# Performance work log

Measured on AMD Instinct MI355X. Metric: run time of the kernel, lower is better.

The kernel has to match this reference:

```python
import jax, jax.numpy as jnp
import numpy as np

E = 1024   # embedding_dim
H = 16     # heads
W = 1024   # lag / seq length
B = 4      # batch
D = E // H # head dim


def setup_inputs() -> dict:
    key = jax.random.key(0)
    ks = jax.random.split(key, 5)
    scale = E ** -0.5
    return {
        "x":   jax.random.normal(ks[0], (3, B, E, W), dtype=jnp.float32),
        "L_Q": jax.random.normal(ks[1], (E, E), dtype=jnp.float32) * scale,
        "L_K": jax.random.normal(ks[2], (E, E), dtype=jnp.float32) * scale,
        "L_V": jax.random.normal(ks[3], (E, E), dtype=jnp.float32) * scale,
        "M":   jax.random.normal(ks[4], (E, E), dtype=jnp.float32) * (1.0 / (2 * E)) ** 0.5,
        "b":   jnp.zeros((E, 1), dtype=jnp.float32),
    }


def reference(x, L_Q, L_K, L_V, M, b):
    # x: [3, B, E, W] channels-first; x[0]=K input, x[1]=Q input, x[2]=V input
    K = jnp.einsum('ef,bfw->bew', L_K, x[0])
    Q = jnp.einsum('ef,bfw->bew', L_Q, x[1])
    V = jnp.einsum('ef,bfw->bew', L_V, x[2])
    # reshape to [B, H, D, W]
    Kv = K.reshape(B, H, D, W)
    Qv = Q.reshape(B, H, D, W)
    Vv = V.reshape(B, H, D, W)
    # scores[b,h,q,k] = Q_v^T @ K_v
    scores = jnp.einsum('bhdq,bhdk->bhqk', Qv, Kv)
    # causal mask: -inf for q > k (strictly lower triangle), added BEFORE softmax
    q_idx = jnp.arange(W)[:, None]
    k_idx = jnp.arange(W)[None, :]
    mask = jnp.where(q_idx > k_idx, -jnp.inf, 0.0).astype(scores.dtype)
    scores = scores + mask
    # NON-STANDARD: softmax over the QUERY axis (dim=-2), then scale
    attn = jax.nn.softmax(scores, axis=-2) / (E ** 0.5)
    # V_v @ scores: [B,H,D,W] @ [B,H,W,W] -> [B,H,D,W]
    out = jnp.einsum('bhdq,bhqk->bhdk', Vv, attn).reshape(B, E, W)
    # dense: M @ out + b (dropout identity at inference)
    return jnp.einsum('oe,bew->bow', M, out) + b
```

## Files before the change

### kernel.cpp

```cpp
#include <hip/hip_runtime.h>
#include <stdint.h>
#include <math.h>

#define E_DIM 1024
#define W_DIM 1024
#define EW 1048576L

typedef _Float16 h16;
typedef __attribute__((ext_vector_type(8))) _Float16 h8;
typedef __attribute__((ext_vector_type(4))) float f4;

__device__ __forceinline__ void async_copy16(h16* lds, const h16* g) {
    __builtin_amdgcn_global_load_lds(
        (const __attribute__((address_space(1))) void*)g,
        (__attribute__((address_space(3))) void*)lds, 16, 0, 0);
}

__global__ __launch_bounds__(256) void prep(
    const float* __restrict__ x, const float* __restrict__ LK,
    const float* __restrict__ LQ, const float* __restrict__ LV,
    const float* __restrict__ Mw, h16* __restrict__ xt, h16* __restrict__ wh)
{
    __shared__ float Ts[64][65];
    const int z = blockIdx.z;
    const int t = threadIdx.x;
    if (z < 12) {
        const float* src = x + (long)z * EW;
        h16* dst = xt + (long)z * EW;
        const int e0 = blockIdx.y * 64, w0 = blockIdx.x * 64;
        const int r = t >> 4, c4 = (t & 15) * 4;
        #pragma unroll
        for (int p = 0; p < 4; ++p) {
            float4 v = *reinterpret_cast<const float4*>(src + (long)(e0 + r + p * 16) * W_DIM + w0 + c4);
            Ts[c4 + 0][r + p * 16] = v.x;
            Ts[c4 + 1][r + p * 16] = v.y;
            Ts[c4 + 2][r + p * 16] = v.z;
            Ts[c4 + 3][r + p * 16] = v.w;
        }
        __syncthreads();
        #pragma unroll
        for (int p = 0; p < 4; ++p) {
            int wr = r + p * 16;
            union { h16 h[4]; uint2 u; } o;
            o.h[0] = (h16)Ts[wr][c4 + 0];
            o.h[1] = (h16)Ts[wr][c4 + 1];
            o.h[2] = (h16)Ts[wr][c4 + 2];
            o.h[3] = (h16)Ts[wr][c4 + 3];
            *reinterpret_cast<uint2*>(dst + (long)(w0 + wr) * E_DIM + e0 + c4) = o.u;
        }
    } else {
        const float* srcs[4] = {LK, LQ, LV, Mw};
        const float* s = srcs[z - 12];
        h16* o = wh + (long)(z - 12) * EW;
        long base = ((long)(blockIdx.y * 16 + blockIdx.x)) * 1024 + t;
        #pragma unroll
        for (int k = 0; k < 4; ++k) {
            long i = base + k * 256;
            float4 v = reinterpret_cast<const float4*>(s)[i];
            union { h16 h[4]; uint2 u; } u;
            u.h[0] = (h16)v.x; u.h[1] = (h16)v.y; u.h[2] = (h16)v.z; u.h[3] = (h16)v.w;
            reinterpret_cast<uint2*>(o)[i] = u.u;
        }
    }
}

__global__ __launch_bounds__(256) void gemm_proj3(
    const h16* __restrict__ xh, const h16* __restrict__ Wts,
    h16* __restrict__ KQV)
{
    __shared__ h16 As[128 * 64];
    __shared__ h16 Bs[128 * 64];

    const int t = threadIdx.x;
    const int wave = t >> 6, lane = t & 63;
    const int quad = lane >> 4, l16 = lane & 15;
    const int m0 = blockIdx.y * 128, n0 = blockIdx.x * 128;
    const int wm = (wave >> 1) * 64, wn = (wave & 1) * 64;

    const int proj = blockIdx.z >> 2, bz = blockIdx.z & 3;
    const h16 *A, *Bt; h16* C;
    if (proj == 0)      { A = xh + bz * EW;       Bt = Wts;          C = KQV + bz * EW; }
    else if (proj == 1) { A = xh + (4 + bz) * EW; Bt = Wts + EW;     C = KQV + (4 + bz) * EW; }
    else                { A = Wts + 2 * EW;       Bt = xh + (8 + bz) * EW; C = KQV + (8 + bz) * EW; }

    f4 acc[4][4] = {};

    for (int k0 = 0; k0 < 1024; k0 += 64) {
        __syncthreads();
        #pragma unroll
        for (int j = 0; j < 4; ++j) {
            int g = j * 256 + t, row = g >> 3, cg = (g & 7) ^ (row & 7);
            async_copy16(&As[g * 8], A  + (long)(m0 + row) * E_DIM + k0 + cg * 8);
            async_copy16(&Bs[g * 8], Bt + (long)(n0 + row) * E_DIM + k0 + cg * 8);
        }
        __syncthreads();

        h8 av[4][2], bv[4][2];
        #pragma unroll
        for (int i = 0; i < 4; ++i) {
            int ra = wm + i * 16 + l16, rb = wn + i * 16 + l16;
            #pragma unroll
            for (int c = 0; c < 2; ++c) {
                av[i][c] = *reinterpret_cast<const h8*>(&As[(ra * 8 + ((c * 4 + quad) ^ (l16 & 7))) * 8]);
                bv[i][c] = *reinterpret_cast<const h8*>(&Bs[(rb * 8 + ((c * 4 + quad) ^ (l16 & 7))) * 8]);
            }
        }
        #pragma unroll
        for (int c = 0; c < 2; ++c)
            #pragma unroll
            for (int mt = 0; mt < 4; ++mt)
                #pragma unroll
                for (int nt = 0; nt < 4; ++nt)
                    acc[mt][nt] = __builtin_amdgcn_mfma_f32_16x16x32_f16(av[mt][c], bv[nt][c], acc[mt][nt], 0, 0, 0);
    }

    #pragma unroll
    for (int mt = 0; mt < 4; ++mt)
        #pragma unroll
        for (int i = 0; i < 4; ++i) {
            int m = m0 + wm + mt * 16 + quad * 4 + i;
            #pragma unroll
            for (int nt = 0; nt < 4; ++nt)
                C[(long)m * W_DIM + n0 + wn + nt * 16 + l16] = (h16)acc[mt][nt][i];
        }
}

__global__ __launch_bounds__(256) void gemm_out(
    const h16* __restrict__ A, const h16* __restrict__ Bt,
    float* __restrict__ C, const float* __restrict__ bias)
{
    __shared__ h16 As[64 * 64];
    __shared__ h16 Bs[128 * 64];

    const int t = threadIdx.x;
    const int wave = t >> 6, lane = t & 63;
    const int quad = lane >> 4, l16 = lane & 15;
    const int m0 = blockIdx.y * 64, n0 = blockIdx.x * 128;
    const int wm = (wave >> 1) * 32, wn = (wave & 1) * 64;

    f4 acc[2][4] = {};

    for (int k0 = 0; k0 < 1024; k0 += 64) {
        __syncthreads();
        #pragma unroll
        for (int j = 0; j < 2; ++j) {
            int g = j * 256 + t, row = g >> 3, cg = (g & 7) ^ (row & 7);
            async_copy16(&As[g * 8], A + (long)(m0 + row) * E_DIM + k0 + cg * 8);
        }
        #pragma unroll
        for (int j = 0; j < 4; ++j) {
            int g = j * 256 + t, row = g >> 3, cg = (g & 7) ^ (row & 7);
            async_copy16(&Bs[g * 8], Bt + (long)(n0 + row) * E_DIM + k0 + cg * 8);
        }
        __syncthreads();

        h8 av[2][2], bv[4][2];
        #pragma unroll
        for (int c = 0; c < 2; ++c) {
            #pragma unroll
            for (int mt = 0; mt < 2; ++mt) {
                int r = wm + mt * 16 + l16;
                av[mt][c] = *reinterpret_cast<const h8*>(&As[(r * 8 + ((c * 4 + quad) ^ (l16 & 7))) * 8]);
            }
            #pragma unroll
            for (int nt = 0; nt < 4; ++nt) {
                int r = wn + nt * 16 + l16;
                bv[nt][c] = *reinterpret_cast<const h8*>(&Bs[(r * 8 + ((c * 4 + quad) ^ (l16 & 7))) * 8]);
            }
        }
        #pragma unroll
        for (int c = 0; c < 2; ++c)
            #pragma unroll
            for (int mt = 0; mt < 2; ++mt)
                #pragma unroll
                for (int nt = 0; nt < 4; ++nt)
                    acc[mt][nt] = __builtin_amdgcn_mfma_f32_16x16x32_f16(av[mt][c], bv[nt][c], acc[mt][nt], 0, 0, 0);
    }

    #pragma unroll
    for (int mt = 0; mt < 2; ++mt)
        #pragma unroll
        for (int i = 0; i < 4; ++i) {
            int m = m0 + wm + mt * 16 + quad * 4 + i;
            float bv_ = bias ? bias[m] : 0.f;
            #pragma unroll
            for (int nt = 0; nt < 4; ++nt) {
                int n = n0 + wn + nt * 16 + l16;
                C[(long)(n >> 10) * EW + (long)m * W_DIM + (n & 1023)] = acc[mt][nt][i] + bv_;
            }
        }
}

__global__ __launch_bounds__(256) void attn_mfma(
    const h16* __restrict__ Kt, const h16* __restrict__ Qt,
    const h16* __restrict__ V, h16* __restrict__ AoT)
{
    __shared__ h16 Qs[2][64 * 64];
    __shared__ h16 Vs[2][64 * 64];
    __shared__ h16 Ps[4][16 * 72];

    const int t = threadIdx.x, wave = t >> 6, lane = t & 63;
    const int quad = lane >> 4, l16 = lane & 15;
    const int b = blockIdx.y >> 4, h = blockIdx.y & 15;
    const int kt = 15 - blockIdx.x;
    const int kbase = kt * 64 + wave * 16;
    const int kcol = kbase + l16;

    const h16* Ktb = Kt + (long)b * EW + h * 64;
    const h16* Qtb = Qt + (long)b * EW + h * 64;
    const h16* Vb  = V  + (long)b * EW + (long)(h * 64) * W_DIM;
    h16* Pw = &Ps[wave][0];

    h8 kb0 = *reinterpret_cast<const h8*>(Ktb + (long)kcol * E_DIM + quad * 8);
    h8 kb1 = *reinterpret_cast<const h8*>(Ktb + (long)kcol * E_DIM + 32 + quad * 8);

    #pragma unroll
    for (int j = 0; j < 2; ++j) {
        int g = j * 256 + t, row = g >> 3, cg = (g & 7) ^ (row & 7);
        async_copy16(&Qs[0][g * 8], Qtb + (long)row * E_DIM + cg * 8);
        async_copy16(&Vs[0][g * 8], Vb + (long)row * W_DIM + cg * 8);
    }

    float mrow = -1e30f, lsum = 0.f;
    f4 O[4] = {};

    for (int it = 0; it <= kt; ++it) {
        const int q0 = it * 64;
        __syncthreads();
        if (it < kt) {
            int nb = (it + 1) & 1, q1 = q0 + 64;
            #pragma unroll
            for (int j = 0; j < 2; ++j) {
                int g = j * 256 + t, row = g >> 3, cg = (g & 7) ^ (row & 7);
                async_copy16(&Qs[nb][g * 8], Qtb + (long)(q1 + row) * E_DIM + cg * 8);
                async_copy16(&Vs[nb][g * 8], Vb + (long)row * W_DIM + q1 + cg * 8);
            }
        }
        const h16* qs = Qs[it & 1];
        const h16* vs = Vs[it & 1];

        f4 S[4];
        #pragma unroll
        for (int nt = 0; nt < 4; ++nt) {
            int row = nt * 16 + l16;
            h8 a0 = *reinterpret_cast<const h8*>(&qs[(row * 8 + (quad ^ (l16 & 7))) * 8]);
            h8 a1 = *reinterpret_cast<const h8*>(&qs[(row * 8 + ((4 + quad) ^ (l16 & 7))) * 8]);
            f4 s = {};
            s = __builtin_amdgcn_mfma_f32_16x16x32_f16(a0, kb0, s, 0, 0, 0);
            s = __builtin_amdgcn_mfma_f32_16x16x32_f16(a1, kb1, s, 0, 0, 0);
            S[nt] = s;
        }

        if (it == kt) {
            #pragma unroll
            for (int nt = 0; nt < 4; ++nt)
                #pragma unroll
                for (int i = 0; i < 4; ++i)
                    if (q0 + nt * 16 + quad * 4 + i > kcol) S[nt][i] = -1e30f;
        }

        float mx = -1e30f;
        #pragma unroll
        for (int nt = 0; nt < 4; ++nt)
            #pragma unroll
            for (int i = 0; i < 4; ++i) mx = fmaxf(mx, S[nt][i]);
        mx = fmaxf(mx, __shfl_xor(mx, 16));
        mx = fmaxf(mx, __shfl_xor(mx, 32));
        float nm = fmaxf(mrow, mx);
        float al = __expf(mrow - nm);
        mrow = nm;

        float ts = 0.f;
        #pragma unroll
        for (int nt = 0; nt < 4; ++nt)
            #pragma unroll
            for (int i = 0; i < 4; ++i) {
                float p = __expf(S[nt][i] - nm);
                S[nt][i] = p;
                ts += p;
            }
        ts += __shfl_xor(ts, 16);
        ts += __shfl_xor(ts, 32);
        lsum = lsum * al + ts;
        #pragma unroll
        for (int dt = 0; dt < 4; ++dt)
            #pragma unroll
            for (int i = 0; i < 4; ++i) O[dt][i] *= al;

        #pragma unroll
        for (int nt = 0; nt < 4; ++nt) {
            union { h16 hh[4]; uint2 u2; } p;
            p.hh[0] = (h16)S[nt][0]; p.hh[1] = (h16)S[nt][1];
            p.hh[2] = (h16)S[nt][2]; p.hh[3] = (h16)S[nt][3];
            *reinterpret_cast<uint2*>(Pw + l16 * 72 + nt * 16 + quad * 4) = p.u2;
        }
        asm volatile("" ::: "memory");

        #pragma unroll
        for (int c = 0; c < 2; ++c) {
            h8 pb = *reinterpret_cast<const h8*>(Pw + l16 * 72 + c * 32 + quad * 8);
            #pragma unroll
            for (int dt = 0; dt < 4; ++dt) {
                int r = dt * 16 + l16;
                h8 va = *reinterpret_cast<const h8*>(&vs[(r * 8 + ((c * 4 + quad) ^ (l16 & 7))) * 8]);
                O[dt] = __builtin_amdgcn_mfma_f32_16x16x32_f16(va, pb, O[dt], 0, 0, 0);
            }
        }
    }

    float inv = 0.03125f / lsum;
    #pragma unroll
    for (int dt = 0; dt < 4; ++dt) {
        union { h16 hh[4]; uint2 u2; } p;
        #pragma unroll
        for (int i = 0; i < 4; ++i) p.hh[i] = (h16)(O[dt][i] * inv);
        *reinterpret_cast<uint2*>(Pw + l16 * 72 + dt * 16 + quad * 4) = p.u2;
    }
    asm volatile("" ::: "memory");
    #pragma unroll
    for (int j = 0; j < 2; ++j) {
        uint4 vv = *reinterpret_cast<const uint4*>(Pw + l16 * 72 + quad * 16 + j * 8);
        *reinterpret_cast<uint4*>(AoT + (long)b * EW + (long)(kbase + l16) * E_DIM
                                  + h * 64 + quad * 16 + j * 8) = vv;
    }
}

extern "C" void kernel_launch(void* const* d_in, const int* in_sizes, int n_in,
                              void* d_out, int out_size, void* d_ws, size_t ws_size,
                              hipStream_t stream)
{
    const float* x  = (const float*)d_in[0];
    const float* LQ = (const float*)d_in[1];
    const float* LK = (const float*)d_in[2];
    const float* LV = (const float*)d_in[3];
    const float* Mw = (const float*)d_in[4];
    const float* bb = (const float*)d_in[5];
    float* out = (float*)d_out;
    h16* ws = (h16*)d_ws;

    h16* xh  = ws;
    h16* LKh = ws + 12 * EW;
    h16* Mh  = ws + 15 * EW;
    h16* Kp  = ws + 16 * EW;
    h16* Qp  = ws + 20 * EW;
    h16* Vp  = ws + 24 * EW;
    h16* Ao  = ws + 28 * EW;

    dim3 blk(256);
    prep<<<dim3(16, 16, 16), blk, 0, stream>>>(x, LK, LQ, LV, Mw, xh, LKh);
    gemm_proj3<<<dim3(8, 8, 12), blk, 0, stream>>>(xh, LKh, Kp);
    attn_mfma<<<dim3(16, 64), blk, 0, stream>>>(Kp, Qp, Vp, Ao);
    gemm_out<<<dim3(32, 16), blk, 0, stream>>>(Mh, Ao, out, bb);
}
```

Baseline: 205.7 us.

## Restructure attention into 512-thread blocks with lazy rescale, and swizzle projection GEMM grid

The attention kernel now uses 512-thread blocks covering 128 keys each, with per-wave skipping of fully masked query tiles. Key-tile order is permuted per head to balance the causal load, and online-softmax rescaling runs only when the max grows by more than a threshold. It also switches to exp2 with split partial sums, XOR-swizzles the P staging buffer instead of padding it, and raises MFMA wave priority. Separately, the projection GEMM remaps block indices so blocks scheduled together share operands. The lazy rescale relies on fp16 P staying in range, and the bigger blocks cut occupancy granularity.

Measured after the change: 190.8 us. 1.08x faster.

```diff
diff --git a/kernel.cpp b/kernel.cpp
--- a/kernel.cpp
+++ b/kernel.cpp
@@ -74,10 +74,15 @@
     const int t = threadIdx.x;
     const int wave = t >> 6, lane = t & 63;
     const int quad = lane >> 4, l16 = lane & 15;
-    const int m0 = blockIdx.y * 128, n0 = blockIdx.x * 128;
+
+    const int lin = (int)blockIdx.x + ((int)blockIdx.y << 3) + ((int)blockIdx.z << 6);
+    const int swz = (lin & 7) * 96 + (lin >> 3);
+    const int bx = swz & 7, by = (swz >> 3) & 7, zz = swz >> 6;
+
+    const int m0 = by * 128, n0 = bx * 128;
     const int wm = (wave >> 1) * 64, wn = (wave & 1) * 64;
 
-    const int proj = blockIdx.z >> 2, bz = blockIdx.z & 3;
+    const int proj = zz >> 2, bz = zz & 3;
     const h16 *A, *Bt; h16* C;
     if (proj == 0)      { A = xh + bz * EW;       Bt = Wts;          C = KQV + bz * EW; }
     else if (proj == 1) { A = xh + (4 + bz) * EW; Bt = Wts + EW;     C = KQV + (4 + bz) * EW; }
@@ -191,55 +196,58 @@
         }
 }
 
-__global__ __launch_bounds__(256) void attn_mfma(
+__global__ __launch_bounds__(512) void attn_mfma(
     const h16* __restrict__ Kt, const h16* __restrict__ Qt,
     const h16* __restrict__ V, h16* __restrict__ AoT)
 {
     __shared__ h16 Qs[2][64 * 64];
     __shared__ h16 Vs[2][64 * 64];
-    __shared__ h16 Ps[4][16 * 72];
+    __shared__ h16 Ps[8][16 * 64];
 
     const int t = threadIdx.x, wave = t >> 6, lane = t & 63;
     const int quad = lane >> 4, l16 = lane & 15;
-    const int b = blockIdx.y >> 4, h = blockIdx.y & 15;
-    const int kt = 15 - blockIdx.x;
-    const int kbase = kt * 64 + wave * 16;
-    const int kcol = kbase + l16;
-
-    const h16* Ktb = Kt + (long)b * EW + h * 64;
-    const h16* Qtb = Qt + (long)b * EW + h * 64;
-    const h16* Vb  = V  + (long)b * EW + (long)(h * 64) * W_DIM;
+    const int y = blockIdx.y;
+    const int b = y >> 4, h = y & 15;
+    const int cxor = (y & 7) ^ (((y >> 5) & 1) ? 7 : 0);
+    const int ktb = (int)blockIdx.x ^ cxor;
+    const int nit = 2 * ktb + 2;
+    const int kwave = ktb * 128 + wave * 16;
+    const int kc = kwave + l16;
+
+    const h16* Ktb_ = Kt + (long)b * EW + h * 64;
+    const h16* Qtb  = Qt + (long)b * EW + h * 64;
+    const h16* Vb   = V  + (long)b * EW + (long)(h * 64) * W_DIM;
     h16* Pw = &Ps[wave][0];
 
-    h8 kb0 = *reinterpret_cast<const h8*>(Ktb + (long)kcol * E_DIM + quad * 8);
-    h8 kb1 = *reinterpret_cast<const h8*>(Ktb + (long)kcol * E_DIM + 32 + quad * 8);
-
-    #pragma unroll
-    for (int j = 0; j < 2; ++j) {
-        int g = j * 256 + t, row = g >> 3, cg = (g & 7) ^ (row & 7);
-        async_copy16(&Qs[0][g * 8], Qtb + (long)row * E_DIM + cg * 8);
-        async_copy16(&Vs[0][g * 8], Vb + (long)row * W_DIM + cg * 8);
-    }
-
-    float mrow = -1e30f, lsum = 0.f;
+    h8 kb0 = *reinterpret_cast<const h8*>(Ktb_ + (long)kc * E_DIM + quad * 8);
+    h8 kb1 = *reinterpret_cast<const h8*>(Ktb_ + (long)kc * E_DIM + 32 + quad * 8);
+
+    {
+        int row = t >> 3, cg = (t & 7) ^ (row & 7);
+        async_copy16(&Qs[0][t * 8], Qtb + (long)row * E_DIM + cg * 8);
+        async_copy16(&Vs[0][t * 8], Vb + (long)row * W_DIM + cg * 8);
+    }
+
+    const float L2E = 1.442695041f;
+    float mr = -1e30f, ls = 0.f;
     f4 O[4] = {};
 
-    for (int it = 0; it <= kt; ++it) {
+    for (int it = 0; it < nit; ++it) {
         const int q0 = it * 64;
         __syncthreads();
-        if (it < kt) {
-            int nb = (it + 1) & 1, q1 = q0 + 64;
-            #pragma unroll
-            for (int j = 0; j < 2; ++j) {
-                int g = j * 256 + t, row = g >> 3, cg = (g & 7) ^ (row & 7);
-                async_copy16(&Qs[nb][g * 8], Qtb + (long)(q1 + row) * E_DIM + cg * 8);
-                async_copy16(&Vs[nb][g * 8], Vb + (long)row * W_DIM + q1 + cg * 8);
-            }
-        }
+        if (it + 1 < nit) {
+            const int nb = (it + 1) & 1, q1 = q0 + 64;
+            int row = t >> 3, cg = (t & 7) ^ (row & 7);
+            async_copy16(&Qs[nb][t * 8], Qtb + (long)(q1 + row) * E_DIM + cg * 8);
+            async_copy16(&Vs[nb][t * 8], Vb + (long)row * W_DIM + q1 + cg * 8);
+        }
+        if (q0 > kwave + 15) continue;
+
         const h16* qs = Qs[it & 1];
         const h16* vs = Vs[it & 1];
 
         f4 S[4];
+        __builtin_amdgcn_s_setprio(1);
         #pragma unroll
         for (int nt = 0; nt < 4; ++nt) {
             int row = nt * 16 + l16;
@@ -250,55 +258,66 @@
             s = __builtin_amdgcn_mfma_f32_16x16x32_f16(a1, kb1, s, 0, 0, 0);
             S[nt] = s;
         }
-
-        if (it == kt) {
+        __builtin_amdgcn_s_setprio(0);
+
+        if (it >= 2 * ktb) {
             #pragma unroll
             for (int nt = 0; nt < 4; ++nt)
                 #pragma unroll
                 for (int i = 0; i < 4; ++i)
-                    if (q0 + nt * 16 + quad * 4 + i > kcol) S[nt][i] = -1e30f;
+                    if (q0 + nt * 16 + quad * 4 + i > kc) S[nt][i] = -1e30f;
         }
 
         float mx = -1e30f;
         #pragma unroll
-        for (int nt = 0; nt < 4; ++nt)
-            #pragma unroll
-            for (int i = 0; i < 4; ++i) mx = fmaxf(mx, S[nt][i]);
+        for (int nt = 0; nt < 4; ++nt) {
+            float t0 = fmaxf(fmaxf(S[nt][0], S[nt][1]), fmaxf(S[nt][2], S[nt][3]));
+            mx = fmaxf(mx, t0);
+        }
         mx = fmaxf(mx, __shfl_xor(mx, 16));
         mx = fmaxf(mx, __shfl_xor(mx, 32));
-        float nm = fmaxf(mrow, mx);
-        float al = __expf(mrow - nm);
-        mrow = nm;
-
-        float ts = 0.f;
+
+        if (__any(mx - mr > 8.f)) {
+            float nm = fmaxf(mr, mx);
+            float al = exp2f((mr - nm) * L2E);
+            mr = nm;
+            ls *= al;
+            #pragma unroll
+            for (int dt = 0; dt < 4; ++dt)
+                #pragma unroll
+                for (int i = 0; i < 4; ++i) O[dt][i] *= al;
+        }
+
+        const float mc = mr * L2E;
+        float tsa = 0.f, tsb = 0.f;
         #pragma unroll
         for (int nt = 0; nt < 4; ++nt)
             #pragma unroll
             for (int i = 0; i < 4; ++i) {
-                float p = __expf(S[nt][i] - nm);
+                float p = exp2f(fmaf(S[nt][i], L2E, -mc));
                 S[nt][i] = p;
-                ts += p;
-            }
+                if (i & 1) tsb += p; else tsa += p;
+            }
+        float ts = tsa + tsb;
         ts += __shfl_xor(ts, 16);
         ts += __shfl_xor(ts, 32);
-        lsum = lsum * al + ts;
-        #pragma unroll
-        for (int dt = 0; dt < 4; ++dt)
-            #pragma unroll
-            for (int i = 0; i < 4; ++i) O[dt][i] *= al;
+        ls += ts;
 
         #pragma unroll
         for (int nt = 0; nt < 4; ++nt) {
-            union { h16 hh[4]; uint2 u2; } p;
-            p.hh[0] = (h16)S[nt][0]; p.hh[1] = (h16)S[nt][1];
-            p.hh[2] = (h16)S[nt][2]; p.hh[3] = (h16)S[nt][3];
-            *reinterpret_cast<uint2*>(Pw + l16 * 72 + nt * 16 + quad * 4) = p.u2;
+            int sg = ((nt * 2 + (quad >> 1)) ^ (l16 & 7)) * 8 + (quad & 1) * 4;
+            union { h16 hh[4]; uint2 u2; } u0;
+            #pragma unroll
+            for (int i = 0; i < 4; ++i) u0.hh[i] = (h16)S[nt][i];
+            *reinterpret_cast<uint2*>(Pw + l16 * 64 + sg) = u0.u2;
         }
         asm volatile("" ::: "memory");
 
+        __builtin_amdgcn_s_setprio(1);
         #pragma unroll
         for (int c = 0; c < 2; ++c) {
-            h8 pb = *reinterpret_cast<const h8*>(Pw + l16 * 72 + c * 32 + quad * 8);
+            int sg = ((c * 4 + quad) ^ (l16 & 7)) * 8;
+            h8 pb = *reinterpret_cast<const h8*>(Pw + l16 * 64 + sg);
             #pragma unroll
             for (int dt = 0; dt < 4; ++dt) {
                 int r = dt * 16 + l16;
@@ -306,21 +325,24 @@
                 O[dt] = __builtin_amdgcn_mfma_f32_16x16x32_f16(va, pb, O[dt], 0, 0, 0);
             }
         }
-    }
-
-    float inv = 0.03125f / lsum;
+        __builtin_amdgcn_s_setprio(0);
+    }
+
+    const float inv = 0.03125f / ls;
     #pragma unroll
     for (int dt = 0; dt < 4; ++dt) {
-        union { h16 hh[4]; uint2 u2; } p;
-        #pragma unroll
-        for (int i = 0; i < 4; ++i) p.hh[i] = (h16)(O[dt][i] * inv);
-        *reinterpret_cast<uint2*>(Pw + l16 * 72 + dt * 16 + quad * 4) = p.u2;
+        int sg = ((dt * 2 + (quad >> 1)) ^ (l16 & 7)) * 8 + (quad & 1) * 4;
+        union { h16 hh[4]; uint2 u2; } u0;
+        #pragma unroll
+        for (int i = 0; i < 4; ++i) u0.hh[i] = (h16)(O[dt][i] * inv);
+        *reinterpret_cast<uint2*>(Pw + l16 * 64 + sg) = u0.u2;
     }
     asm volatile("" ::: "memory");
     #pragma unroll
     for (int j = 0; j < 2; ++j) {
-        uint4 vv = *reinterpret_cast<const uint4*>(Pw + l16 * 72 + quad * 16 + j * 8);
-        *reinterpret_cast<uint4*>(AoT + (long)b * EW + (long)(kbase + l16) * E_DIM
+        int sg = ((quad * 2 + j) ^ (l16 & 7)) * 8;
+        uint4 vv = *reinterpret_cast<const uint4*>(Pw + l16 * 64 + sg);
+        *reinterpret_cast<uint4*>(AoT + (long)b * EW + (long)(kwave + l16) * E_DIM
                                   + h * 64 + quad * 16 + j * 8) = vv;
     }
 }
@@ -349,6 +371,6 @@
     dim3 blk(256);
     prep<<<dim3(16, 16, 16), blk, 0, stream>>>(x, LK, LQ, LV, Mw, xh, LKh);
     gemm_proj3<<<dim3(8, 8, 12), blk, 0, stream>>>(xh, LKh, Kp);
-    attn_mfma<<<dim3(16, 64), blk, 0, stream>>>(Kp, Qp, Vp, Ao);
+    attn_mfma<<<dim3(8, 64), dim3(512), 0, stream>>>(Kp, Qp, Vp, Ao);
     gemm_out<<<dim3(32, 16), blk, 0, stream>>>(Mh, Ao, out, bb);
 }
```
